# Performance work log

Measured on AMD Instinct MI355X. Metric: run time of the kernel, lower is better.

Reference implementation:

```python
import jax, jax.numpy as jnp
import numpy as np

B, S, D, DH = 2, 2048, 1024, 64
H = D // DH
EPS = 1e-6

def rms_norm(x):
    # flax RMSNorm, use_scale=False: x / sqrt(mean(x^2) + eps)
    return x * jax.lax.rsqrt(jnp.mean(jnp.square(x), axis=-1, keepdims=True) + EPS)

def setup_inputs() -> dict:
    key = jax.random.key(0)
    ks = jax.random.split(key, 6)
    std = (1.0 / D) ** 0.5
    x = jax.random.normal(ks[0], (B, S, D), dtype=jnp.float32)
    Wq = jax.random.normal(ks[1], (D, D), dtype=jnp.float32) * std
    Wk = jax.random.normal(ks[2], (D, D), dtype=jnp.float32) * std
    Wv = jax.random.normal(ks[3], (D, D), dtype=jnp.float32) * std
    # output_proj is zero-initialized in the original; use small random so
    # backward through it is non-trivial for kernel correctness testing.
    Wo = jax.random.normal(ks[4], (D, D), dtype=jnp.float32) * std
    mask = jnp.tril(jnp.ones((S, S), dtype=bool))[None, None]  # causal [1,1,S,S]
    return {"x": x, "Wq": Wq, "Wk": Wk, "Wv": Wv, "Wo": Wo, "mask": mask}

def reference(x, Wq, Wk, Wv, Wo, mask):
    scale = (1.0 / DH) ** 0.5
    q = (x @ Wq).reshape(B, S, H, DH).transpose(0, 2, 1, 3)  # [B,H,S,DH]
    k = (x @ Wk).reshape(B, S, H, DH).transpose(0, 2, 1, 3)
    v = (x @ Wv).reshape(B, S, H, DH).transpose(0, 2, 1, 3)
    q = rms_norm(q)
    k = rms_norm(k)
    scores = jnp.einsum('bhsd,bhtd->bhst', q, k) * scale
    scores = jnp.where(mask, scores, jnp.finfo(scores.dtype).min)
    probs = jax.nn.softmax(scores, axis=-1)
    out = jnp.einsum('bhst,bhtd->bhsd', probs, v)
    out = out.transpose(0, 2, 1, 3).reshape(B, S, D)
    return out @ Wo
```

## Files before the change

kernel.cpp:

```cpp
#include <hip/hip_runtime.h>
#include <stdint.h>


typedef __attribute__((ext_vector_type(8))) short s16x8;
typedef __attribute__((ext_vector_type(4))) float fx4;
typedef __attribute__((ext_vector_type(4))) unsigned int ux4;
typedef __attribute__((ext_vector_type(2))) unsigned int ux2;

__device__ __forceinline__ unsigned short f2bf(float x) {
  unsigned u = __builtin_bit_cast(unsigned, x);
  u += 0x7fffu + ((u >> 16) & 1u);
  return (unsigned short)(u >> 16);
}
__device__ __forceinline__ float bf2f(unsigned short h) {
  return __builtin_bit_cast(float, (unsigned)h << 16);
}

__device__ __forceinline__ void gload_lds16(const void* g, void* l) {
  __builtin_amdgcn_global_load_lds(
      (const __attribute__((address_space(1))) unsigned int*)g,
      (__attribute__((address_space(3))) unsigned int*)l, 16, 0, 0);
}

__global__ void k_conv_bf16(const float* __restrict__ X,
                            unsigned short* __restrict__ Y, int n4) {
  int stride = gridDim.x * blockDim.x;
  for (int i = blockIdx.x * blockDim.x + threadIdx.x; i < n4; i += stride) {
    fx4 v = *(const fx4*)(X + (size_t)i * 4);
    ux2 o;
    o[0] = (unsigned)f2bf(v[0]) | ((unsigned)f2bf(v[1]) << 16);
    o[1] = (unsigned)f2bf(v[2]) | ((unsigned)f2bf(v[3]) << 16);
    *(ux2*)(Y + (size_t)i * 4) = o;
  }
}

__global__ void k_transpose_w(const float* __restrict__ W0, const float* __restrict__ W1,
                              const float* __restrict__ W2, const float* __restrict__ W3,
                              unsigned short* __restrict__ T0, unsigned short* __restrict__ T1,
                              unsigned short* __restrict__ T2, unsigned short* __restrict__ T3) {
  const float* W = blockIdx.z == 0 ? W0 : blockIdx.z == 1 ? W1 : blockIdx.z == 2 ? W2 : W3;
  unsigned short* T = blockIdx.z == 0 ? T0 : blockIdx.z == 1 ? T1 : blockIdx.z == 2 ? T2 : T3;
  __shared__ float t[32][33];
  int bx = blockIdx.x * 32, by = blockIdx.y * 32;
  int tx = threadIdx.x, ty = threadIdx.y;
#pragma unroll
  for (int i = 0; i < 32; i += 8)
    t[ty + i][tx] = W[(size_t)(by + ty + i) * 1024 + bx + tx];
  __syncthreads();
#pragma unroll
  for (int i = 0; i < 32; i += 8)
    T[(size_t)(bx + ty + i) * 1024 + by + tx] = f2bf(t[tx][ty + i]);
}

template <int MODE>
__global__ __launch_bounds__(256, 2)
void k_gemm_bt(const unsigned short* __restrict__ A,
               const unsigned short* __restrict__ W0,
               const unsigned short* __restrict__ W1,
               const unsigned short* __restrict__ W2,
               void* __restrict__ Cptr, int ldc,
               unsigned short* __restrict__ qn, unsigned short* __restrict__ kn,
               unsigned short* __restrict__ vb) {
  __shared__ unsigned short As[128 * 64];
  __shared__ unsigned short Bs[128 * 64];
  const int tid = threadIdx.x;
  const int w = tid >> 6, l = tid & 63;
  const int lr = l & 15, lg = l >> 4;
  const int wm = w >> 1, wn = w & 1;
  const int m0 = blockIdx.x * 128;
  const int nt = blockIdx.y;
  const unsigned short* Bt = (nt < 8) ? W0 : (nt < 16) ? W1 : W2;
  const int n0 = (nt & 7) * 128;

  fx4 acc[4][4] = {};

  const int srow = w * 8 + (l >> 3);
  const int skb  = ((l & 7) ^ (l >> 3)) * 8;
  const unsigned short* aB = A  + (size_t)(m0 + srow) * 1024 + skb;
  const unsigned short* bB = Bt + (size_t)(n0 + srow) * 1024 + skb;
  unsigned short* aD = &As[w * 512];
  unsigned short* bD = &Bs[w * 512];
  const int rdswz = (l & 7) << 4;

  for (int kt = 0; kt < 1024; kt += 64) {
    __syncthreads();
#pragma unroll
    for (int j = 0; j < 4; ++j) {
      gload_lds16(aB + j * 32768 + kt, aD + j * 2048);
      gload_lds16(bB + j * 32768 + kt, bD + j * 2048);
    }
    __syncthreads();
#pragma unroll
    for (int ks = 0; ks < 2; ++ks) {
      const int kb = (ks * 64 + lg * 16) ^ rdswz;
      s16x8 af[4], bf[4];
#pragma unroll
      for (int mf = 0; mf < 4; ++mf)
        af[mf] = *(const s16x8*)((const char*)As + (wm * 64 + mf * 16 + lr) * 128 + kb);
#pragma unroll
      for (int nf = 0; nf < 4; ++nf)
        bf[nf] = *(const s16x8*)((const char*)Bs + (wn * 64 + nf * 16 + lr) * 128 + kb);
#pragma unroll
      for (int mf = 0; mf < 4; ++mf)
#pragma unroll
        for (int nf = 0; nf < 4; ++nf)
          acc[mf][nf] = __builtin_amdgcn_mfma_f32_16x16x32_bf16(af[mf], bf[nf], acc[mf][nf], 0, 0, 0);
    }
  }

  if (MODE == 1) {
    const int gn = nt * 128 + wn * 64;
    const int gm = m0 + wm * 64;
#pragma unroll
    for (int mf = 0; mf < 4; ++mf)
#pragma unroll
      for (int r = 0; r < 4; ++r) {
        int row = gm + mf * 16 + lg * 4 + r;
        float* C = (float*)Cptr + (size_t)row * ldc + gn;
#pragma unroll
        for (int nf = 0; nf < 4; ++nf) C[nf * 16 + lr] = acc[mf][nf][r];
      }
  } else {
    const int tz = nt >> 3;
    const int h  = ((nt & 7) << 1) | wn;
    const int gm = m0 + wm * 64;
    unsigned short* base = tz == 0 ? qn : tz == 1 ? kn : vb;
    const float cmul = (tz == 0) ? 0.18033688f : 1.0f;
#pragma unroll
    for (int mf = 0; mf < 4; ++mf)
#pragma unroll
      for (int r = 0; r < 4; ++r) {
        int m = gm + mf * 16 + lg * 4 + r;
        float ss = 0.f;
#pragma unroll
        for (int nf = 0; nf < 4; ++nf) ss += acc[mf][nf][r] * acc[mf][nf][r];
        ss += __shfl_xor(ss, 1);
        ss += __shfl_xor(ss, 2);
        ss += __shfl_xor(ss, 4);
        ss += __shfl_xor(ss, 8);
        float scale = (tz == 2) ? 1.0f : rsqrtf(ss * (1.0f / 64.0f) + 1e-6f) * cmul;
        int b = m >> 11, s = m & 2047;
        unsigned short* dst = base + ((size_t)(((b << 4) + h) * 2048 + s)) * 64;
#pragma unroll
        for (int nf = 0; nf < 4; ++nf)
          dst[nf * 16 + lr] = f2bf(acc[mf][nf][r] * scale);
      }
  }
}

__global__ __launch_bounds__(128, 2)
void k_attn(const unsigned short* __restrict__ Q,
            const unsigned short* __restrict__ K,
            const unsigned short* __restrict__ V,
            unsigned short* __restrict__ O) {
  __shared__ unsigned short Ks[2][64 * 64];
  __shared__ unsigned short Vt[2][64 * 64];
  __shared__ unsigned short Ps[2][32 * 64];

  const int id = blockIdx.x;
  const int bh = id & 31;
  const int pp = id >> 5;
  const int q2 = pp & 15;
  const int bse = (q2 & 1) ? 15 - (q2 >> 1) : (q2 >> 1);
  const int tq = (pp >> 4) ? 31 - bse : bse;
  const int q0 = tq * 64;
  const int tid = threadIdx.x;
  const int w = tid >> 6, l = tid & 63;
  const int lr = l & 15, lg = l >> 4;
  const int b = bh >> 4, h = bh & 15;
  const int qw = q0 + w * 32;

  const unsigned short* Kb = K + (size_t)bh * 2048 * 64;
  const unsigned short* Vb = V + (size_t)bh * 2048 * 64;
  const unsigned short* Qb = Q + ((size_t)bh * 2048 + qw) * 64;

  s16x8 aq[2][2];
#pragma unroll
  for (int mf = 0; mf < 2; ++mf)
#pragma unroll
    for (int ks = 0; ks < 2; ++ks)
      aq[mf][ks] = *(const s16x8*)(Qb + (mf * 16 + lr) * 64 + ks * 32 + lg * 8);

  fx4 oacc[2][4] = {};
  float lsum[2][4] = {{0.f, 0.f, 0.f, 0.f}, {0.f, 0.f, 0.f, 0.f}};

  const int ksub = l >> 3;
  const int kskb = ((l & 7) ^ ksub) * 8;
  const int vc = tid & 31;
  const int vg = tid >> 5;
  const int kvlo = (vc & 15) + (vc >> 4) * 32;
  const int rdswz = (lr & 7) << 4;
  const float FMAX = 11.5415603f;
  const int ntl = tq + 1;

  ux4 va0, va1, va2, va3;
#pragma unroll
  for (int j = 0; j < 4; ++j)
    gload_lds16(Kb + (size_t)(j * 16 + w * 8 + ksub) * 64 + kskb,
                &Ks[0][(j * 16 + w * 8) * 64]);
  va0 = *(const ux4*)(Vb + (size_t)kvlo * 64 + vg * 16);
  va1 = *(const ux4*)(Vb + (size_t)kvlo * 64 + vg * 16 + 8);
  va2 = *(const ux4*)(Vb + (size_t)(kvlo + 16) * 64 + vg * 16);
  va3 = *(const ux4*)(Vb + (size_t)(kvlo + 16) * 64 + vg * 16 + 8);
  {
    union { ux4 v; unsigned short u[8]; } a0, a1, a2, a3;
    a0.v = va0; a1.v = va1; a2.v = va2; a3.v = va3;
#pragma unroll
    for (int i = 0; i < 8; ++i) {
      int dh = vg * 16 + i;
      *(unsigned*)((char*)&Vt[0][0] + dh * 128 + ((vc * 4) ^ ((i & 7) << 4))) =
          (unsigned)a0.u[i] | ((unsigned)a2.u[i] << 16);
      *(unsigned*)((char*)&Vt[0][0] + (dh + 8) * 128 + ((vc * 4) ^ ((i & 7) << 4))) =
          (unsigned)a1.u[i] | ((unsigned)a3.u[i] << 16);
    }
  }
  __syncthreads();

#pragma unroll 1
  for (int t = 0; t < ntl; ++t) {
    const int cur = t & 1;
    const int kv0 = t * 64;
    const bool pre = (t + 1 < ntl);
    if (pre) {
      const int kvn = kv0 + 64;
#pragma unroll
      for (int j = 0; j < 4; ++j)
        gload_lds16(Kb + (size_t)(kvn + j * 16 + w * 8 + ksub) * 64 + kskb,
                    &Ks[cur ^ 1][(j * 16 + w * 8) * 64]);
      va0 = *(const ux4*)(Vb + (size_t)(kvn + kvlo) * 64 + vg * 16);
      va1 = *(const ux4*)(Vb + (size_t)(kvn + kvlo) * 64 + vg * 16 + 8);
      va2 = *(const ux4*)(Vb + (size_t)(kvn + kvlo + 16) * 64 + vg * 16);
      va3 = *(const ux4*)(Vb + (size_t)(kvn + kvlo + 16) * 64 + vg * 16 + 8);
    }
    fx4 sc[2][4] = {};
    __builtin_amdgcn_s_setprio(1);
#pragma unroll
    for (int ks = 0; ks < 2; ++ks) {
      const int kb = (ks * 64 + lg * 16) ^ rdswz;
#pragma unroll
      for (int nf = 0; nf < 4; ++nf) {
        s16x8 bk = *(const s16x8*)((const char*)&Ks[cur][0] + (nf * 16 + lr) * 128 + kb);
#pragma unroll
        for (int mf = 0; mf < 2; ++mf)
          sc[mf][nf] = __builtin_amdgcn_mfma_f32_16x16x32_bf16(aq[mf][ks], bk, sc[mf][nf], 0, 0, 0);
      }
    }
    __builtin_amdgcn_s_setprio(0);
    if (t == ntl - 1) {
#pragma unroll
      for (int mf = 0; mf < 2; ++mf)
#pragma unroll
        for (int nf = 0; nf < 4; ++nf)
#pragma unroll
          for (int r = 0; r < 4; ++r) {
            int gq = qw + mf * 16 + lg * 4 + r;
            int gk = kv0 + nf * 16 + lr;
            if (gk > gq) sc[mf][nf][r] = -3.0e38f;
          }
    }
    char* pw = (char*)&Ps[w][0];
#pragma unroll
    for (int mf = 0; mf < 2; ++mf)
#pragma unroll
      for (int r = 0; r < 4; ++r) {
        float p0 = __builtin_amdgcn_exp2f(sc[mf][0][r] - FMAX);
        float p1 = __builtin_amdgcn_exp2f(sc[mf][1][r] - FMAX);
        float p2 = __builtin_amdgcn_exp2f(sc[mf][2][r] - FMAX);
        float p3 = __builtin_amdgcn_exp2f(sc[mf][3][r] - FMAX);
        lsum[mf][r] += (p0 + p1) + (p2 + p3);
        int row = mf * 16 + lg * 4 + r;
        char* pb = pw + row * 128;
        int swz = (row & 7) << 4;
        *(unsigned*)(pb + ((4 * lr) ^ swz))      = (unsigned)f2bf(p0) | ((unsigned)f2bf(p1) << 16);
        *(unsigned*)(pb + ((64 + 4 * lr) ^ swz)) = (unsigned)f2bf(p2) | ((unsigned)f2bf(p3) << 16);
      }
    __builtin_amdgcn_s_setprio(1);
#pragma unroll
    for (int ks = 0; ks < 2; ++ks) {
      s16x8 pa[2], bv[4];
#pragma unroll
      for (int mf = 0; mf < 2; ++mf) {
        int row = mf * 16 + lr;
        pa[mf] = *(const s16x8*)(pw + row * 128 + ((ks * 64 + lg * 16) ^ ((row & 7) << 4)));
      }
#pragma unroll
      for (int nf = 0; nf < 4; ++nf) {
        int row = nf * 16 + lr;
        bv[nf] = *(const s16x8*)((const char*)&Vt[cur][0] + row * 128 +
                                 ((ks * 64 + lg * 16) ^ ((row & 7) << 4)));
      }
#pragma unroll
      for (int mf = 0; mf < 2; ++mf)
#pragma unroll
        for (int nf = 0; nf < 4; ++nf)
          oacc[mf][nf] = __builtin_amdgcn_mfma_f32_16x16x32_bf16(pa[mf], bv[nf], oacc[mf][nf], 0, 0, 0);
    }
    __builtin_amdgcn_s_setprio(0);
    if (pre) {
      union { ux4 v; unsigned short u[8]; } a0, a1, a2, a3;
      a0.v = va0; a1.v = va1; a2.v = va2; a3.v = va3;
#pragma unroll
      for (int i = 0; i < 8; ++i) {
        int dh = vg * 16 + i;
        *(unsigned*)((char*)&Vt[cur ^ 1][0] + dh * 128 + ((vc * 4) ^ ((i & 7) << 4))) =
            (unsigned)a0.u[i] | ((unsigned)a2.u[i] << 16);
        *(unsigned*)((char*)&Vt[cur ^ 1][0] + (dh + 8) * 128 + ((vc * 4) ^ ((i & 7) << 4))) =
            (unsigned)a1.u[i] | ((unsigned)a3.u[i] << 16);
      }
    }
    __syncthreads();
  }

#pragma unroll
  for (int mf = 0; mf < 2; ++mf)
#pragma unroll
    for (int r = 0; r < 4; ++r) {
      float s = lsum[mf][r];
      s += __shfl_xor(s, 1);
      s += __shfl_xor(s, 2);
      s += __shfl_xor(s, 4);
      s += __shfl_xor(s, 8);
      float inv = 1.0f / s;
      int gq = qw + mf * 16 + lg * 4 + r;
      unsigned short* orow = O + ((size_t)(b * 2048 + gq)) * 1024 + h * 64;
#pragma unroll
      for (int nf = 0; nf < 4; ++nf)
        orow[nf * 16 + lr] = f2bf(oacc[mf][nf][r] * inv);
    }
}

extern "C" void kernel_launch(void* const* d_in, const int* in_sizes, int n_in,
                              void* d_out, int out_size, void* d_ws, size_t ws_size,
                              hipStream_t stream) {
  const float* x  = (const float*)d_in[0];
  const float* Wq = (const float*)d_in[1];
  const float* Wk = (const float*)d_in[2];
  const float* Wv = (const float*)d_in[3];
  const float* Wo = (const float*)d_in[4];

  char* ws = (char*)d_ws;
  unsigned short* xb   = (unsigned short*)(ws);
  unsigned short* WqT  = (unsigned short*)(ws + (8ll  << 20));
  unsigned short* WkT  = (unsigned short*)(ws + (10ll << 20));
  unsigned short* WvT  = (unsigned short*)(ws + (12ll << 20));
  unsigned short* WoT  = (unsigned short*)(ws + (14ll << 20));
  unsigned short* qn   = (unsigned short*)(ws + (16ll << 20));
  unsigned short* kn   = (unsigned short*)(ws + (24ll << 20));
  unsigned short* vb   = (unsigned short*)(ws + (32ll << 20));
  unsigned short* attn = (unsigned short*)(ws + (40ll << 20));

  k_conv_bf16<<<1024, 256, 0, stream>>>(x, xb, 4096 * 1024 / 4);
  k_transpose_w<<<dim3(32, 32, 4), dim3(32, 8), 0, stream>>>(Wq, Wk, Wv, Wo, WqT, WkT, WvT, WoT);
  k_gemm_bt<2><<<dim3(32, 24), 256, 0, stream>>>(xb, WqT, WkT, WvT, nullptr, 0, qn, kn, vb);
  k_attn<<<1024, 128, 0, stream>>>(qn, kn, vb, attn);
  k_gemm_bt<1><<<dim3(32, 8), 256, 0, stream>>>(attn, WoT, WoT, WoT, d_out, 1024, nullptr, nullptr, nullptr);
}
```

Before: 117.9 us.

## Balance causal attention work with fixed-length blocks and split-KV merge

Each attention block now does a fixed number of KV tiles, 16 or 17, instead of a count that depends on its query tile. The non-half block first processes the short tile p fully and writes it out, then starts the long tile 31-p. The half block finishes the rest of that long tile's KV range and writes partial fp32 O and row sums, which a new merge kernel combines. This removes load imbalance from causal triangular work, at the cost of an extra kernel launch, fp32 partial traffic, and a mid-loop Q reload.

Result: faster. 110.9 us (-5.9%).

```diff
diff --git a/kernel.cpp b/kernel.cpp
--- a/kernel.cpp
+++ b/kernel.cpp
@@ -152,37 +152,25 @@
 void k_attn(const unsigned short* __restrict__ Q,
             const unsigned short* __restrict__ K,
             const unsigned short* __restrict__ V,
-            unsigned short* __restrict__ O) {
+            unsigned short* __restrict__ O,
+            float* __restrict__ pO,
+            float* __restrict__ pL) {
   __shared__ unsigned short Ks[2][64 * 64];
   __shared__ unsigned short Vt[2][64 * 64];
   __shared__ unsigned short Ps[2][32 * 64];
 
   const int id = blockIdx.x;
-  const int bh = id & 31;
-  const int pp = id >> 5;
-  const int q2 = pp & 15;
-  const int bse = (q2 & 1) ? 15 - (q2 >> 1) : (q2 >> 1);
-  const int tq = (pp >> 4) ? 31 - bse : bse;
-  const int q0 = tq * 64;
+  const int bh = id >> 5;
+  const int c  = id & 31;
+  const int p  = c >> 1, half = c & 1;
   const int tid = threadIdx.x;
   const int w = tid >> 6, l = tid & 63;
   const int lr = l & 15, lg = l >> 4;
   const int b = bh >> 4, h = bh & 15;
-  const int qw = q0 + w * 32;
 
   const unsigned short* Kb = K + (size_t)bh * 2048 * 64;
   const unsigned short* Vb = V + (size_t)bh * 2048 * 64;
-  const unsigned short* Qb = Q + ((size_t)bh * 2048 + qw) * 64;
-
-  s16x8 aq[2][2];
-#pragma unroll
-  for (int mf = 0; mf < 2; ++mf)
-#pragma unroll
-    for (int ks = 0; ks < 2; ++ks)
-      aq[mf][ks] = *(const s16x8*)(Qb + (mf * 16 + lr) * 64 + ks * 32 + lg * 8);
-
-  fx4 oacc[2][4] = {};
-  float lsum[2][4] = {{0.f, 0.f, 0.f, 0.f}, {0.f, 0.f, 0.f, 0.f}};
+  const unsigned short* Qh = Q + (size_t)bh * 2048 * 64;
 
   const int ksub = l >> 3;
   const int kskb = ((l & 7) ^ ksub) * 8;
@@ -191,17 +179,32 @@
   const int kvlo = (vc & 15) + (vc >> 4) * 32;
   const int rdswz = (lr & 7) << 4;
   const float FMAX = 11.5415603f;
-  const int ntl = tq + 1;
+
+  const int NS = half ? 16 : 17;
+  int tile = half ? (31 - p) : p;
+  int qw = tile * 64 + w * 32;
+
+  s16x8 aq[2][2];
+#pragma unroll
+  for (int mf = 0; mf < 2; ++mf)
+#pragma unroll
+    for (int ks = 0; ks < 2; ++ks)
+      aq[mf][ks] = *(const s16x8*)(Qh + (size_t)(qw + mf * 16 + lr) * 64 + ks * 32 + lg * 8);
+
+  fx4 oacc[2][4] = {};
+  float lsum[2][4] = {{0.f, 0.f, 0.f, 0.f}, {0.f, 0.f, 0.f, 0.f}};
+
+  int kvt = half ? (16 - p) : 0;
 
   ux4 va0, va1, va2, va3;
 #pragma unroll
   for (int j = 0; j < 4; ++j)
-    gload_lds16(Kb + (size_t)(j * 16 + w * 8 + ksub) * 64 + kskb,
+    gload_lds16(Kb + (size_t)(kvt * 64 + j * 16 + w * 8 + ksub) * 64 + kskb,
                 &Ks[0][(j * 16 + w * 8) * 64]);
-  va0 = *(const ux4*)(Vb + (size_t)kvlo * 64 + vg * 16);
-  va1 = *(const ux4*)(Vb + (size_t)kvlo * 64 + vg * 16 + 8);
-  va2 = *(const ux4*)(Vb + (size_t)(kvlo + 16) * 64 + vg * 16);
-  va3 = *(const ux4*)(Vb + (size_t)(kvlo + 16) * 64 + vg * 16 + 8);
+  va0 = *(const ux4*)(Vb + (size_t)(kvt * 64 + kvlo) * 64 + vg * 16);
+  va1 = *(const ux4*)(Vb + (size_t)(kvt * 64 + kvlo) * 64 + vg * 16 + 8);
+  va2 = *(const ux4*)(Vb + (size_t)(kvt * 64 + kvlo + 16) * 64 + vg * 16);
+  va3 = *(const ux4*)(Vb + (size_t)(kvt * 64 + kvlo + 16) * 64 + vg * 16 + 8);
   {
     union { ux4 v; unsigned short u[8]; } a0, a1, a2, a3;
     a0.v = va0; a1.v = va1; a2.v = va2; a3.v = va3;
@@ -217,12 +220,46 @@
   __syncthreads();
 
 #pragma unroll 1
-  for (int t = 0; t < ntl; ++t) {
-    const int cur = t & 1;
-    const int kv0 = t * 64;
-    const bool pre = (t + 1 < ntl);
+  for (int s = 0; s < NS; ++s) {
+    if (!half && s == p + 1) {
+#pragma unroll
+      for (int mf = 0; mf < 2; ++mf)
+#pragma unroll
+        for (int r = 0; r < 4; ++r) {
+          float ssum = lsum[mf][r];
+          ssum += __shfl_xor(ssum, 1);
+          ssum += __shfl_xor(ssum, 2);
+          ssum += __shfl_xor(ssum, 4);
+          ssum += __shfl_xor(ssum, 8);
+          float inv = 1.0f / ssum;
+          int gq = qw + mf * 16 + lg * 4 + r;
+          unsigned short* orow = O + ((size_t)(b * 2048 + gq)) * 1024 + h * 64;
+#pragma unroll
+          for (int nf = 0; nf < 4; ++nf)
+            orow[nf * 16 + lr] = f2bf(oacc[mf][nf][r] * inv);
+        }
+#pragma unroll
+      for (int mf = 0; mf < 2; ++mf) {
+#pragma unroll
+        for (int nf = 0; nf < 4; ++nf) oacc[mf][nf] = fx4{0.f, 0.f, 0.f, 0.f};
+#pragma unroll
+        for (int r = 0; r < 4; ++r) lsum[mf][r] = 0.f;
+      }
+      tile = 31 - p;
+      qw = tile * 64 + w * 32;
+#pragma unroll
+      for (int mf = 0; mf < 2; ++mf)
+#pragma unroll
+        for (int ks = 0; ks < 2; ++ks)
+          aq[mf][ks] = *(const s16x8*)(Qh + (size_t)(qw + mf * 16 + lr) * 64 + ks * 32 + lg * 8);
+    }
+    const int cur = s & 1;
+    const int kv0 = kvt * 64;
+    const bool pre = (s + 1 < NS);
+    int nkvt = kvt + 1;
+    if (!half && s == p) nkvt = 0;
     if (pre) {
-      const int kvn = kv0 + 64;
+      const int kvn = nkvt * 64;
 #pragma unroll
       for (int j = 0; j < 4; ++j)
         gload_lds16(Kb + (size_t)(kvn + j * 16 + w * 8 + ksub) * 64 + kskb,
@@ -246,7 +283,8 @@
       }
     }
     __builtin_amdgcn_s_setprio(0);
-    if (t == ntl - 1) {
+    const bool diag = half ? (s == 15) : (s == p);
+    if (diag) {
 #pragma unroll
       for (int mf = 0; mf < 2; ++mf)
 #pragma unroll
@@ -308,25 +346,48 @@
             (unsigned)a1.u[i] | ((unsigned)a3.u[i] << 16);
       }
     }
+    kvt = nkvt;
     __syncthreads();
   }
 
+  const int slot = ((bh * 16 + p) * 2 + half);
 #pragma unroll
   for (int mf = 0; mf < 2; ++mf)
 #pragma unroll
     for (int r = 0; r < 4; ++r) {
-      float s = lsum[mf][r];
-      s += __shfl_xor(s, 1);
-      s += __shfl_xor(s, 2);
-      s += __shfl_xor(s, 4);
-      s += __shfl_xor(s, 8);
-      float inv = 1.0f / s;
-      int gq = qw + mf * 16 + lg * 4 + r;
-      unsigned short* orow = O + ((size_t)(b * 2048 + gq)) * 1024 + h * 64;
-#pragma unroll
-      for (int nf = 0; nf < 4; ++nf)
-        orow[nf * 16 + lr] = f2bf(oacc[mf][nf][r] * inv);
-    }
+      float ssum = lsum[mf][r];
+      ssum += __shfl_xor(ssum, 1);
+      ssum += __shfl_xor(ssum, 2);
+      ssum += __shfl_xor(ssum, 4);
+      ssum += __shfl_xor(ssum, 8);
+      int row = w * 32 + mf * 16 + lg * 4 + r;
+      float* po = pO + ((size_t)slot * 64 + row) * 64;
+#pragma unroll
+      for (int nf = 0; nf < 4; ++nf) po[nf * 16 + lr] = oacc[mf][nf][r];
+      if (lr == 0) pL[slot * 64 + row] = ssum;
+    }
+}
+
+__global__ __launch_bounds__(256)
+void k_merge(const float* __restrict__ pO, const float* __restrict__ pL,
+             unsigned short* __restrict__ O) {
+  int gid = blockIdx.x * 256 + threadIdx.x;
+  int row = gid >> 4;
+  int quad = gid & 15;
+  int slot = row >> 6;
+  int r = row & 63;
+  int bh = slot >> 4, p = slot & 15;
+  fx4 va = *(const fx4*)(pO + ((size_t)(slot * 2) * 64 + r) * 64 + quad * 4);
+  fx4 vb = *(const fx4*)(pO + ((size_t)(slot * 2 + 1) * 64 + r) * 64 + quad * 4);
+  float inv = 1.0f / (pL[(slot * 2) * 64 + r] + pL[(slot * 2 + 1) * 64 + r]);
+  int tile = 31 - p;
+  int b = bh >> 4, h = bh & 15;
+  int s = tile * 64 + r;
+  unsigned short* o = O + ((size_t)(b * 2048 + s)) * 1024 + h * 64 + quad * 4;
+  ux2 out;
+  out[0] = (unsigned)f2bf((va[0] + vb[0]) * inv) | ((unsigned)f2bf((va[1] + vb[1]) * inv) << 16);
+  out[1] = (unsigned)f2bf((va[2] + vb[2]) * inv) | ((unsigned)f2bf((va[3] + vb[3]) * inv) << 16);
+  *(ux2*)o = out;
 }
 
 extern "C" void kernel_launch(void* const* d_in, const int* in_sizes, int n_in,
@@ -348,10 +409,13 @@
   unsigned short* kn   = (unsigned short*)(ws + (24ll << 20));
   unsigned short* vb   = (unsigned short*)(ws + (32ll << 20));
   unsigned short* attn = (unsigned short*)(ws + (40ll << 20));
+  float* pO            = (float*)(ws + (48ll << 20));
+  float* pL            = (float*)(ws + (64ll << 20));
 
   k_conv_bf16<<<1024, 256, 0, stream>>>(x, xb, 4096 * 1024 / 4);
   k_transpose_w<<<dim3(32, 32, 4), dim3(32, 8), 0, stream>>>(Wq, Wk, Wv, Wo, WqT, WkT, WvT, WoT);
   k_gemm_bt<2><<<dim3(32, 24), 256, 0, stream>>>(xb, WqT, WkT, WvT, nullptr, 0, qn, kn, vb);
-  k_attn<<<1024, 128, 0, stream>>>(qn, kn, vb, attn);
+  k_attn<<<1024, 128, 0, stream>>>(qn, kn, vb, attn, pO, pL);
+  k_merge<<<2048, 256, 0, stream>>>(pO, pL, attn);
   k_gemm_bt<1><<<dim3(32, 8), 256, 0, stream>>>(attn, WoT, WoT, WoT, d_out, 1024, nullptr, nullptr, nullptr);
 }
```
